# Kernel optimization log

Hardware: AMD Instinct MI355X
Metric: run time of the kernel (lower is better)

The kernel has to match this reference:

```python
import jax, jax.numpy as jnp
import numpy as np

N = 50000   # nodes
E = 800000  # edges
F_IN, F_HID, F_OUT = 128, 96, 40


def setup_inputs() -> dict:
    key = jax.random.key(0)
    ks = jax.random.split(key, 9)
    x = jax.random.normal(ks[0], (N, F_IN), dtype=jnp.float32)
    edge_index = jax.random.randint(ks[1], (2, E), 0, N, dtype=jnp.int32)
    def lin(k, fi, fo):
        s = 1.0 / np.sqrt(fi)
        return jax.random.uniform(k, (fi, fo), jnp.float32, -s, s)
    W1 = lin(ks[2], F_IN, F_HID)
    b1 = jnp.zeros((F_HID,), jnp.float32)
    W2 = lin(ks[3], F_HID, F_HID)
    b2 = jnp.zeros((F_HID,), jnp.float32)
    Wout = lin(ks[4], F_HID, F_OUT)
    bout = jnp.zeros((F_OUT,), jnp.float32)
    return {"x": x, "edge_index": edge_index, "W1": W1, "b1": b1,
            "W2": W2, "b2": b2, "Wout": Wout, "bout": bout}


def _gcn_norm(edge_index, n):
    # add self-loops, symmetric degree normalization (PyG GCNConv default)
    loops = jnp.arange(n, dtype=edge_index.dtype)
    src = jnp.concatenate([edge_index[0], loops])
    dst = jnp.concatenate([edge_index[1], loops])
    deg = jax.ops.segment_sum(jnp.ones_like(dst, dtype=jnp.float32), dst,
                              num_segments=n)
    dinv = jnp.where(deg > 0, jax.lax.rsqrt(deg), 0.0)
    norm = dinv[src] * dinv[dst]   # [E+N]
    return src, dst, norm


def _gcn_layer(h, src, dst, norm, W, b, n):
    # linear transform, then normalized scatter-add aggregation, then bias
    h = h @ W                                 # [N, Fout]
    msg = h[src] * norm[:, None]              # gather + scale
    agg = jax.ops.segment_sum(msg, dst, num_segments=n)
    return agg + b


def reference(x, edge_index, W1, b1, W2, b2, Wout, bout):
    n = x.shape[0]
    src, dst, norm = _gcn_norm(edge_index, n)
    h = jax.nn.relu(_gcn_layer(x, src, dst, norm, W1, b1, n))
    h = jax.nn.relu(_gcn_layer(h, src, dst, norm, W2, b2, n))
    return h @ Wout + bout
```

## Files before the change

### kernel.cpp

```cpp
#include <hip/hip_runtime.h>
#include <hip/hip_fp16.h>

#define N_NODES 50000
#define N_EDGES 800000
#define F_INN   128
#define F_HID   96
#define F_OUTT  40
#define SLOTS   64

typedef _Float16 half8 __attribute__((ext_vector_type(8)));
typedef float    floatx4 __attribute__((ext_vector_type(4)));

template <int FI, typename TIN, bool SCALE>
__device__ __forceinline__ void mfma_gemm_body(
        const TIN* __restrict__ X, const __half* __restrict__ BTg,
        const float* __restrict__ dinv, float4* __restrict__ Th4, int n, int bx) {
    __shared__ __half BTl[96 * 136];
    __half* OUTl = BTl;
    int tid = threadIdx.x;
    {
        const int4* s = reinterpret_cast<const int4*>(BTg);
        int4* d = reinterpret_cast<int4*>(BTl);
        for (int i = tid; i < 96 * 136 / 8; i += 256) d[i] = s[i];
    }
    __syncthreads();

    int lane = tid & 63, w = tid >> 6;
    int lm = lane & 15, q = lane >> 4;
    int base = bx * 64 + w * 16;
    int node = base + lm;
    int nclamp = min(node, n - 1);
    const TIN* Xrow = X + (size_t)nclamp * FI;

    floatx4 cf[6];
    #pragma unroll
    for (int t = 0; t < 6; ++t) cf[t] = (floatx4){0.f, 0.f, 0.f, 0.f};

    constexpr int KS = FI / 32;
    #pragma unroll
    for (int ks = 0; ks < KS; ++ks) {
        half8 bv;
        if constexpr (sizeof(TIN) == 4) {
            const float4* xr = reinterpret_cast<const float4*>(Xrow + 32 * ks + q * 8);
            float4 f0 = xr[0], f1 = xr[1];
            union { half8 v; __half2 h[4]; } b;
            b.h[0] = __floats2half2_rn(f0.x, f0.y);
            b.h[1] = __floats2half2_rn(f0.z, f0.w);
            b.h[2] = __floats2half2_rn(f1.x, f1.y);
            b.h[3] = __floats2half2_rn(f1.z, f1.w);
            bv = b.v;
        } else {
            bv = *reinterpret_cast<const half8*>(Xrow + 32 * ks + q * 8);
        }
        #pragma unroll
        for (int t = 0; t < 6; ++t) {
            half8 a = *reinterpret_cast<const half8*>(
                &BTl[(t * 16 + lm) * 136 + q * 8 + 32 * ks]);
            cf[t] = __builtin_amdgcn_mfma_f32_16x16x32_f16(a, bv, cf[t], 0, 0, 0);
        }
    }

    float dv = 1.0f;
    if constexpr (SCALE) dv = dinv[nclamp];

    __syncthreads();

    __half* orow = OUTl + (w * 16 + lm) * 104;
    #pragma unroll
    for (int t = 0; t < 6; ++t) {
        union { int2 i2; __half2 h[2]; } u;
        u.h[0] = __floats2half2_rn(dv * cf[t][0], dv * cf[t][1]);
        u.h[1] = __floats2half2_rn(dv * cf[t][2], dv * cf[t][3]);
        *reinterpret_cast<int2*>(&orow[t * 16 + q * 4]) = u.i2;
    }
    #pragma unroll
    for (int R = 0; R < 3; ++R) {
        int nl = lane >> 2, c = (lane & 3) + 4 * R;
        float4 v = *reinterpret_cast<const float4*>(&OUTl[(w * 16 + nl) * 104 + c * 8]);
        int gn = base + nl;
        if (gn < n) Th4[(size_t)gn * 12 + c] = v;
    }
}

__global__ __launch_bounds__(256) void count_gemm1_kernel(
        const int* __restrict__ dst, int* __restrict__ cnt, int* __restrict__ rank,
        int e, const float* __restrict__ X, const __half* __restrict__ BT1,
        float4* __restrict__ Th4, int n, int nCB) {
    if ((int)blockIdx.x < nCB) {
        int i = blockIdx.x * 512 + threadIdx.x;
        int j = i + 256;
        bool bi = i < e, bj = j < e;
        int di = 0, dj = 0, ri, rj;
        if (bi) di = dst[i];
        if (bj) dj = dst[j];
        if (bi) ri = atomicAdd(&cnt[di], 1);
        if (bj) rj = atomicAdd(&cnt[dj], 1);
        if (bi) rank[i] = ri;
        if (bj) rank[j] = rj;
    } else {
        mfma_gemm_body<F_INN, float, false>(X, BT1, nullptr, Th4, n, blockIdx.x - nCB);
    }
}

template <int FI, typename TIN, bool SCALE>
__global__ __launch_bounds__(256) void mfma_gemm_kernel(
        const TIN* __restrict__ X, const __half* __restrict__ BTg,
        const float* __restrict__ dinv, float4* __restrict__ Th4, int n) {
    mfma_gemm_body<FI, TIN, SCALE>(X, BTg, dinv, Th4, n, blockIdx.x);
}

__global__ void wt_kernel(const float* __restrict__ W1, const float* __restrict__ W2,
                          __half* __restrict__ BT1, __half* __restrict__ BT2) {
    int i = blockIdx.x * 256 + threadIdx.x;
    if (i < 96 * 128) {
        int j = i / 128, k = i - j * 128;
        BT1[j * 136 + k] = __float2half(W1[k * 96 + j]);
    } else if (i < 96 * 128 + 96 * 96) {
        int t = i - 96 * 128;
        int j = t / 96, k = t - j * 96;
        BT2[j * 136 + k] = __float2half(W2[k * 96 + j]);
    }
}

__global__ __launch_bounds__(256) void fill_scale_kernel(
        const int* __restrict__ src, const int* __restrict__ dst,
        const int* __restrict__ rank, int* __restrict__ csr_pad,
        const int* __restrict__ cnt, float* __restrict__ dinv,
        float4* __restrict__ Th4, int e, int n, int nFB) {
    if ((int)blockIdx.x < nFB) {
        int i = blockIdx.x * 256 + threadIdx.x;
        if (i >= e) return;
        int r = rank[i];
        if (r < SLOTS) csr_pad[dst[i] * SLOTS + r] = src[i];
    } else {
        int i = (blockIdx.x - nFB) * 256 + threadIdx.x;
        if (i < n) dinv[i] = rsqrtf((float)min(cnt[i], SLOTS) + 1.0f);
        if (i >= n * 12) return;
        int node = i / 12;
        float s = rsqrtf((float)min(cnt[node], SLOTS) + 1.0f);
        union { float4 f4; __half2 h[4]; } u;
        u.f4 = Th4[i];
        #pragma unroll
        for (int q = 0; q < 4; ++q) {
            float2 t = __half22float2(u.h[q]);
            u.h[q] = __floats2half2_rn(s * t.x, s * t.y);
        }
        Th4[i] = u.f4;
    }
}

__global__ __launch_bounds__(256) void agg_kernel(
        const __half2* __restrict__ T, const int* __restrict__ cnt,
        const int* __restrict__ csr_pad, const float* __restrict__ dinv,
        const float* __restrict__ bias, __half2* __restrict__ H, int n) {
    int lane = threadIdx.x & 63;
    int node = __builtin_amdgcn_readfirstlane(blockIdx.x * 4 + (threadIdx.x >> 6));
    if (node >= n) return;
    int fl = min(lane, 47);

    float dn = dinv[node];
    float2 self = __half22float2(T[(size_t)node * 48 + fl]);
    float accx = self.x, accy = self.y;

    const int* row = csr_pad + (size_t)node * SLOTS;
    int deg = min(cnt[node], SLOTS);
    int idx = 0;
    for (; idx + 8 <= deg; idx += 8) {
        int s[8];
        #pragma unroll
        for (int u = 0; u < 8; ++u) s[u] = row[idx + u];
        float2 f[8];
        #pragma unroll
        for (int u = 0; u < 8; ++u) f[u] = __half22float2(T[(size_t)s[u] * 48 + fl]);
        #pragma unroll
        for (int u = 0; u < 8; ++u) {
            accx += f[u].x;
            accy += f[u].y;
        }
    }
    for (; idx < deg; ++idx) {
        int s = row[idx];
        float2 f = __half22float2(T[(size_t)s * 48 + fl]);
        accx += f.x;
        accy += f.y;
    }
    if (lane < 48) {
        float2 b = reinterpret_cast<const float2*>(bias)[lane];
        float ox = fmaxf(fmaf(dn, accx, b.x), 0.f);
        float oy = fmaxf(fmaf(dn, accy, b.y), 0.f);
        H[(size_t)node * 48 + lane] = __floats2half2_rn(ox, oy);
    }
}

__global__ __launch_bounds__(320) void gemm_out_kernel(
        const __half2* __restrict__ A, const float* __restrict__ W,
        const float* __restrict__ bias, float* __restrict__ C, int n) {
    __shared__ float Wlds[96 * 40];
    int tid = threadIdx.y * 10 + threadIdx.x;
    for (int i = tid; i < 96 * 10; i += 320)
        reinterpret_cast<float4*>(Wlds)[i] = reinterpret_cast<const float4*>(W)[i];
    __syncthreads();

    int j    = threadIdx.x * 4;
    int node = blockIdx.x * 32 + threadIdx.y;
    int nc   = min(node, n - 1);
    const __half2* Ah = A + (size_t)nc * 48;
    float4 acc = make_float4(0.f, 0.f, 0.f, 0.f);
    for (int k2 = 0; k2 < 48; k2 += 2) {
        float2 a01 = __half22float2(Ah[k2]);
        float2 a23 = __half22float2(Ah[k2 + 1]);
        int k = 2 * k2;
        float4 w0 = *reinterpret_cast<const float4*>(Wlds + (k + 0) * 40 + j);
        float4 w1 = *reinterpret_cast<const float4*>(Wlds + (k + 1) * 40 + j);
        float4 w2 = *reinterpret_cast<const float4*>(Wlds + (k + 2) * 40 + j);
        float4 w3 = *reinterpret_cast<const float4*>(Wlds + (k + 3) * 40 + j);
        acc.x += a01.x * w0.x + a01.y * w1.x + a23.x * w2.x + a23.y * w3.x;
        acc.y += a01.x * w0.y + a01.y * w1.y + a23.x * w2.y + a23.y * w3.y;
        acc.z += a01.x * w0.z + a01.y * w1.z + a23.x * w2.z + a23.y * w3.z;
        acc.w += a01.x * w0.w + a01.y * w1.w + a23.x * w2.w + a23.y * w3.w;
    }
    if (node < n) {
        float4 b = *reinterpret_cast<const float4*>(bias + j);
        acc.x += b.x; acc.y += b.y; acc.z += b.z; acc.w += b.w;
        *reinterpret_cast<float4*>(C + (size_t)node * 40 + j) = acc;
    }
}


extern "C" void kernel_launch(void* const* d_in, const int* in_sizes, int n_in,
                              void* d_out, int out_size, void* d_ws, size_t ws_size,
                              hipStream_t stream) {
    const float* x    = (const float*)d_in[0];
    const int*   ei   = (const int*)d_in[1];
    const float* W1   = (const float*)d_in[2];
    const float* b1   = (const float*)d_in[3];
    const float* W2   = (const float*)d_in[4];
    const float* b2   = (const float*)d_in[5];
    const float* Wout = (const float*)d_in[6];
    const float* bout = (const float*)d_in[7];
    float*       out  = (float*)d_out;

    const int* src = ei;
    const int* dst = ei + N_EDGES;

    char* ws = (char*)d_ws;
    size_t off = 0;
    auto alloc = [&](size_t bytes) {
        size_t o = off;
        off = (off + bytes + 511) & ~(size_t)511;
        return (void*)(ws + o);
    };
    int*     cnt       = (int*)    alloc((size_t)N_NODES * sizeof(int));
    float*   dinv      = (float*)  alloc(N_NODES * sizeof(float));
    int*     rank      = (int*)    alloc((size_t)N_EDGES * sizeof(int));
    int*     csr_pad   = (int*)    alloc((size_t)N_NODES * SLOTS * sizeof(int));
    __half*  BT1       = (__half*) alloc((size_t)96 * 136 * sizeof(__half));
    __half*  BT2       = (__half*) alloc((size_t)96 * 136 * sizeof(__half));
    __half2* Th        = (__half2*)alloc((size_t)N_NODES * 48 * sizeof(__half2));
    __half2* Hh        = (__half2*)alloc((size_t)N_NODES * 48 * sizeof(__half2));

    const int CB2 = (N_EDGES + 511) / 512;
    const int FB  = (N_EDGES + 255) / 256;
    const int SB  = (N_NODES * 12 + 255) / 256;
    const int GB  = (N_NODES + 63) / 64;
    const int AB  = (N_NODES + 3) / 4;

    hipMemsetAsync(cnt, 0, (size_t)N_NODES * sizeof(int), stream);
    wt_kernel<<<(96 * 128 + 96 * 96 + 255) / 256, 256, 0, stream>>>(W1, W2, BT1, BT2);

    count_gemm1_kernel<<<CB2 + GB, 256, 0, stream>>>(
        dst, cnt, rank, N_EDGES, x, BT1, (float4*)Th, N_NODES, CB2);

    fill_scale_kernel<<<FB + SB, 256, 0, stream>>>(
        src, dst, rank, csr_pad, cnt, dinv, (float4*)Th, N_EDGES, N_NODES, FB);

    agg_kernel<<<AB, 256, 0, stream>>>(
        Th, cnt, csr_pad, dinv, b1, Hh, N_NODES);

    mfma_gemm_kernel<F_HID, __half, true><<<GB, 256, 0, stream>>>(
        (const __half*)Hh, BT2, dinv, (float4*)Th, N_NODES);
    agg_kernel<<<AB, 256, 0, stream>>>(
        Th, cnt, csr_pad, dinv, b2, Hh, N_NODES);

    gemm_out_kernel<<<(N_NODES + 31) / 32, dim3(10, 32), 0, stream>>>(
        Hh, Wout, bout, out, N_NODES);
}
```

Baseline: 223.7 us.

## Slice feature tables into four 24-wide planes for cache-friendly aggregation

Stores the 96-wide fp16 hidden features as four separate 24-feature slices (node-major within each slice). Every producer and consumer (GEMMs, scale, gemm_out) now indexes the new layout. The aggregation kernel is reorganised so each block handles one slice for a group of 16 nodes, with 5 lanes per node splitting the neighbour list and DPP shifts reducing partial sums. Blocks are interleaved so that each slice's gather working set (about 2.4MB) is more likely to fit in L2 than the full table. The memset is folded into the weight-transpose kernel. Risks are extra index arithmetic, wasted lanes (15 of 16 active), and a more complex reduction.

```diff
diff --git a/kernel.cpp b/kernel.cpp
--- a/kernel.cpp
+++ b/kernel.cpp
@@ -7,6 +7,10 @@
 #define F_HID   96
 #define F_OUTT  40
 #define SLOTS   64
+
+#define SL_HALVES (N_NODES * 24)
+#define SL_F4     (N_NODES * 3)
+#define NGRP      3125
 
 typedef _Float16 half8 __attribute__((ext_vector_type(8)));
 typedef float    floatx4 __attribute__((ext_vector_type(4)));
@@ -30,7 +34,6 @@
     int base = bx * 64 + w * 16;
     int node = base + lm;
     int nclamp = min(node, n - 1);
-    const TIN* Xrow = X + (size_t)nclamp * FI;
 
     floatx4 cf[6];
     #pragma unroll
@@ -41,7 +44,8 @@
     for (int ks = 0; ks < KS; ++ks) {
         half8 bv;
         if constexpr (sizeof(TIN) == 4) {
-            const float4* xr = reinterpret_cast<const float4*>(Xrow + 32 * ks + q * 8);
+            const float4* xr = reinterpret_cast<const float4*>(
+                X + (size_t)nclamp * FI + 32 * ks + q * 8);
             float4 f0 = xr[0], f1 = xr[1];
             union { half8 v; __half2 h[4]; } b;
             b.h[0] = __floats2half2_rn(f0.x, f0.y);
@@ -50,7 +54,11 @@
             b.h[3] = __floats2half2_rn(f1.z, f1.w);
             bv = b.v;
         } else {
-            bv = *reinterpret_cast<const half8*>(Xrow + 32 * ks + q * 8);
+            int c8 = 4 * ks + q;
+            int sl = c8 / 3, of8 = c8 - sl * 3;
+            bv = *reinterpret_cast<const half8*>(
+                reinterpret_cast<const _Float16*>(X) +
+                (size_t)sl * SL_HALVES + (size_t)nclamp * 24 + of8 * 8);
         }
         #pragma unroll
         for (int t = 0; t < 6; ++t) {
@@ -76,9 +84,10 @@
     #pragma unroll
     for (int R = 0; R < 3; ++R) {
         int nl = lane >> 2, c = (lane & 3) + 4 * R;
+        int sl = c / 3, of8 = c - sl * 3;
         float4 v = *reinterpret_cast<const float4*>(&OUTl[(w * 16 + nl) * 104 + c * 8]);
         int gn = base + nl;
-        if (gn < n) Th4[(size_t)gn * 12 + c] = v;
+        if (gn < n) Th4[(size_t)sl * SL_F4 + (size_t)gn * 3 + of8] = v;
     }
 }
 
@@ -109,9 +118,11 @@
     mfma_gemm_body<FI, TIN, SCALE>(X, BTg, dinv, Th4, n, blockIdx.x);
 }
 
-__global__ void wt_kernel(const float* __restrict__ W1, const float* __restrict__ W2,
-                          __half* __restrict__ BT1, __half* __restrict__ BT2) {
+__global__ void wt_zero_kernel(const float* __restrict__ W1, const float* __restrict__ W2,
+                               __half* __restrict__ BT1, __half* __restrict__ BT2,
+                               int* __restrict__ cnt) {
     int i = blockIdx.x * 256 + threadIdx.x;
+    if (i < N_NODES) cnt[i] = 0;
     if (i < 96 * 128) {
         int j = i / 128, k = i - j * 128;
         BT1[j * 136 + k] = __float2half(W1[k * 96 + j]);
@@ -136,7 +147,8 @@
         int i = (blockIdx.x - nFB) * 256 + threadIdx.x;
         if (i < n) dinv[i] = rsqrtf((float)min(cnt[i], SLOTS) + 1.0f);
         if (i >= n * 12) return;
-        int node = i / 12;
+        int rem = i % (n * 3);
+        int node = rem / 3;
         float s = rsqrtf((float)min(cnt[node], SLOTS) + 1.0f);
         union { float4 f4; __half2 h[4]; } u;
         u.f4 = Th4[i];
@@ -149,51 +161,83 @@
     }
 }
 
+template <int N>
+__device__ __forceinline__ float dpp_shl(float x) {
+    return __int_as_float(__builtin_amdgcn_update_dpp(
+        0, __float_as_int(x), 0x100 + N, 0xF, 0xF, true));
+}
+
 __global__ __launch_bounds__(256) void agg_kernel(
-        const __half2* __restrict__ T, const int* __restrict__ cnt,
+        const __half* __restrict__ T, const int* __restrict__ cnt,
         const int* __restrict__ csr_pad, const float* __restrict__ dinv,
-        const float* __restrict__ bias, __half2* __restrict__ H, int n) {
-    int lane = threadIdx.x & 63;
-    int node = __builtin_amdgcn_readfirstlane(blockIdx.x * 4 + (threadIdx.x >> 6));
-    if (node >= n) return;
-    int fl = min(lane, 47);
-
+        const float* __restrict__ bias, __half* __restrict__ H, int n) {
+    int bid = blockIdx.x;
+    int xr = bid & 7, m = bid >> 3;
+    int s  = xr >> 1;
+    int grp = m * 2 + (xr & 1);
+    if (grp >= NGRP) return;
+
+    int tid = threadIdx.x, lane = tid & 63, wid = tid >> 6;
+    int e5 = lane & 15;
+    int e  = e5 / 3;
+    int g  = e5 - e * 3;
+    bool act = e5 < 15;
+
+    int node = grp * 16 + wid * 4 + (lane >> 4);
     float dn = dinv[node];
-    float2 self = __half22float2(T[(size_t)node * 48 + fl]);
-    float accx = self.x, accy = self.y;
-
     const int* row = csr_pad + (size_t)node * SLOTS;
     int deg = min(cnt[node], SLOTS);
-    int idx = 0;
-    for (; idx + 8 <= deg; idx += 8) {
-        int s[8];
+    const _Float16* Ts = reinterpret_cast<const _Float16*>(T) + (size_t)s * SL_HALVES;
+
+    float acc[8];
+    #pragma unroll
+    for (int t = 0; t < 8; ++t) acc[t] = 0.f;
+
+    auto ROUND = [&](int q) {
+        int sn = node; float w = 0.f;
+        if (act) {
+            if (q >= 0 && q < deg) { sn = row[q]; w = 1.f; }
+            else if (q == -1)      { w = 1.f; }
+        }
+        union { half8 v; __half2 h[4]; } u;
+        u.v = *reinterpret_cast<const half8*>(Ts + (size_t)sn * 24 + g * 8);
         #pragma unroll
-        for (int u = 0; u < 8; ++u) s[u] = row[idx + u];
-        float2 f[8];
-        #pragma unroll
-        for (int u = 0; u < 8; ++u) f[u] = __half22float2(T[(size_t)s[u] * 48 + fl]);
-        #pragma unroll
-        for (int u = 0; u < 8; ++u) {
-            accx += f[u].x;
-            accy += f[u].y;
-        }
-    }
-    for (; idx < deg; ++idx) {
-        int s = row[idx];
-        float2 f = __half22float2(T[(size_t)s * 48 + fl]);
-        accx += f.x;
-        accy += f.y;
-    }
-    if (lane < 48) {
-        float2 b = reinterpret_cast<const float2*>(bias)[lane];
-        float ox = fmaxf(fmaf(dn, accx, b.x), 0.f);
-        float oy = fmaxf(fmaf(dn, accy, b.y), 0.f);
-        H[(size_t)node * 48 + lane] = __floats2half2_rn(ox, oy);
+        for (int t = 0; t < 4; ++t) {
+            float2 f = __half22float2(u.h[t]);
+            acc[2 * t]     = fmaf(w, f.x, acc[2 * t]);
+            acc[2 * t + 1] = fmaf(w, f.y, acc[2 * t + 1]);
+        }
+    };
+    int p = -1 + e;
+    do { ROUND(p); ROUND(p + 5); p += 10; } while (__any(act && p < deg));
+
+    float tot[8];
+    #pragma unroll
+    for (int t = 0; t < 8; ++t) {
+        float v1 = acc[t] + dpp_shl<3>(acc[t]);
+        float v2 = v1 + dpp_shl<6>(v1);
+        tot[t] = v2 + dpp_shl<12>(acc[t]);
+    }
+
+    if (e5 < 3) {
+        const float4* bp = reinterpret_cast<const float4*>(bias + s * 24 + e5 * 8);
+        float4 b0 = bp[0], b1 = bp[1];
+        union { int4 i4; __half2 h[4]; } o;
+        o.h[0] = __floats2half2_rn(fmaxf(fmaf(dn, tot[0], b0.x), 0.f),
+                                   fmaxf(fmaf(dn, tot[1], b0.y), 0.f));
+        o.h[1] = __floats2half2_rn(fmaxf(fmaf(dn, tot[2], b0.z), 0.f),
+                                   fmaxf(fmaf(dn, tot[3], b0.w), 0.f));
+        o.h[2] = __floats2half2_rn(fmaxf(fmaf(dn, tot[4], b1.x), 0.f),
+                                   fmaxf(fmaf(dn, tot[5], b1.y), 0.f));
+        o.h[3] = __floats2half2_rn(fmaxf(fmaf(dn, tot[6], b1.z), 0.f),
+                                   fmaxf(fmaf(dn, tot[7], b1.w), 0.f));
+        *reinterpret_cast<int4*>(
+            H + (size_t)s * SL_HALVES + (size_t)node * 24 + e5 * 8) = o.i4;
     }
 }
 
 __global__ __launch_bounds__(320) void gemm_out_kernel(
-        const __half2* __restrict__ A, const float* __restrict__ W,
+        const __half* __restrict__ A, const float* __restrict__ W,
         const float* __restrict__ bias, float* __restrict__ C, int n) {
     __shared__ float Wlds[96 * 40];
     int tid = threadIdx.y * 10 + threadIdx.x;
@@ -204,20 +248,24 @@
     int j    = threadIdx.x * 4;
     int node = blockIdx.x * 32 + threadIdx.y;
     int nc   = min(node, n - 1);
-    const __half2* Ah = A + (size_t)nc * 48;
     float4 acc = make_float4(0.f, 0.f, 0.f, 0.f);
-    for (int k2 = 0; k2 < 48; k2 += 2) {
-        float2 a01 = __half22float2(Ah[k2]);
-        float2 a23 = __half22float2(Ah[k2 + 1]);
-        int k = 2 * k2;
-        float4 w0 = *reinterpret_cast<const float4*>(Wlds + (k + 0) * 40 + j);
-        float4 w1 = *reinterpret_cast<const float4*>(Wlds + (k + 1) * 40 + j);
-        float4 w2 = *reinterpret_cast<const float4*>(Wlds + (k + 2) * 40 + j);
-        float4 w3 = *reinterpret_cast<const float4*>(Wlds + (k + 3) * 40 + j);
-        acc.x += a01.x * w0.x + a01.y * w1.x + a23.x * w2.x + a23.y * w3.x;
-        acc.y += a01.x * w0.y + a01.y * w1.y + a23.x * w2.y + a23.y * w3.y;
-        acc.z += a01.x * w0.z + a01.y * w1.z + a23.x * w2.z + a23.y * w3.z;
-        acc.w += a01.x * w0.w + a01.y * w1.w + a23.x * w2.w + a23.y * w3.w;
+    #pragma unroll
+    for (int c8 = 0; c8 < 12; ++c8) {
+        int sl = c8 / 3, of8 = c8 - sl * 3;
+        union { int4 i4; __half2 h[4]; } u;
+        u.i4 = *reinterpret_cast<const int4*>(
+            A + (size_t)sl * SL_HALVES + (size_t)nc * 24 + of8 * 8);
+        #pragma unroll
+        for (int t = 0; t < 4; ++t) {
+            float2 a = __half22float2(u.h[t]);
+            int k = c8 * 8 + 2 * t;
+            float4 w0 = *reinterpret_cast<const float4*>(Wlds + k * 40 + j);
+            float4 w1 = *reinterpret_cast<const float4*>(Wlds + (k + 1) * 40 + j);
+            acc.x += a.x * w0.x + a.y * w1.x;
+            acc.y += a.x * w0.y + a.y * w1.y;
+            acc.z += a.x * w0.z + a.y * w1.z;
+            acc.w += a.x * w0.w + a.y * w1.w;
+        }
     }
     if (node < n) {
         float4 b = *reinterpret_cast<const float4*>(bias + j);
@@ -250,23 +298,22 @@
         off = (off + bytes + 511) & ~(size_t)511;
         return (void*)(ws + o);
     };
-    int*     cnt       = (int*)    alloc((size_t)N_NODES * sizeof(int));
-    float*   dinv      = (float*)  alloc(N_NODES * sizeof(float));
-    int*     rank      = (int*)    alloc((size_t)N_EDGES * sizeof(int));
-    int*     csr_pad   = (int*)    alloc((size_t)N_NODES * SLOTS * sizeof(int));
-    __half*  BT1       = (__half*) alloc((size_t)96 * 136 * sizeof(__half));
-    __half*  BT2       = (__half*) alloc((size_t)96 * 136 * sizeof(__half));
-    __half2* Th        = (__half2*)alloc((size_t)N_NODES * 48 * sizeof(__half2));
-    __half2* Hh        = (__half2*)alloc((size_t)N_NODES * 48 * sizeof(__half2));
+    int*     cnt     = (int*)    alloc((size_t)N_NODES * sizeof(int));
+    float*   dinv    = (float*)  alloc(N_NODES * sizeof(float));
+    int*     rank    = (int*)    alloc((size_t)N_EDGES * sizeof(int));
+    int*     csr_pad = (int*)    alloc((size_t)N_NODES * SLOTS * sizeof(int));
+    __half*  BT1     = (__half*) alloc((size_t)96 * 136 * sizeof(__half));
+    __half*  BT2     = (__half*) alloc((size_t)96 * 136 * sizeof(__half));
+    __half*  Th      = (__half*) alloc((size_t)N_NODES * 96 * sizeof(__half));
+    __half*  Hh      = (__half*) alloc((size_t)N_NODES * 96 * sizeof(__half));
 
     const int CB2 = (N_EDGES + 511) / 512;
     const int FB  = (N_EDGES + 255) / 256;
     const int SB  = (N_NODES * 12 + 255) / 256;
     const int GB  = (N_NODES + 63) / 64;
-    const int AB  = (N_NODES + 3) / 4;
-
-    hipMemsetAsync(cnt, 0, (size_t)N_NODES * sizeof(int), stream);
-    wt_kernel<<<(96 * 128 + 96 * 96 + 255) / 256, 256, 0, stream>>>(W1, W2, BT1, BT2);
+    const int AGB = ((NGRP + 1) / 2) * 8;
+
+    wt_zero_kernel<<<(N_NODES + 255) / 256, 256, 0, stream>>>(W1, W2, BT1, BT2, cnt);
 
     count_gemm1_kernel<<<CB2 + GB, 256, 0, stream>>>(
         dst, cnt, rank, N_EDGES, x, BT1, (float4*)Th, N_NODES, CB2);
@@ -274,13 +321,11 @@
     fill_scale_kernel<<<FB + SB, 256, 0, stream>>>(
         src, dst, rank, csr_pad, cnt, dinv, (float4*)Th, N_EDGES, N_NODES, FB);
 
-    agg_kernel<<<AB, 256, 0, stream>>>(
-        Th, cnt, csr_pad, dinv, b1, Hh, N_NODES);
+    agg_kernel<<<AGB, 256, 0, stream>>>(Th, cnt, csr_pad, dinv, b1, Hh, N_NODES);
 
     mfma_gemm_kernel<F_HID, __half, true><<<GB, 256, 0, stream>>>(
         (const __half*)Hh, BT2, dinv, (float4*)Th, N_NODES);
-    agg_kernel<<<AB, 256, 0, stream>>>(
-        Th, cnt, csr_pad, dinv, b2, Hh, N_NODES);
+    agg_kernel<<<AGB, 256, 0, stream>>>(Th, cnt, csr_pad, dinv, b2, Hh, N_NODES);
 
     gemm_out_kernel<<<(N_NODES + 31) / 32, dim3(10, 32), 0, stream>>>(
         Hh, Wout, bout, out, N_NODES);
```

Result: slower. 232.6 us (+4.0%).
